# Kernel optimization log

Measured on AMD Instinct MI355X. Metric: run time of the kernel, lower is better.

Reference implementation:

```python
import jax, jax.numpy as jnp
import numpy as np

DIM = 64
WIDTH = 128
INPUT_DIM = 16
N_NODES = 50000
N_EDGES = 100000
N_GRAPHS = 2500
STEPS = 5


def setup_inputs() -> dict:
    key = jax.random.key(0)
    ks = jax.random.split(key, 24)
    d = DIM
    def nrm(i, shape, fan_in):
        return jax.random.normal(ks[i], shape, jnp.float32) / np.float32(np.sqrt(fan_in))
    return {
        "x": jax.random.normal(ks[0], (N_NODES, INPUT_DIM - 1), jnp.float32),
        "z": jax.random.normal(ks[1], (N_NODES,), jnp.float32),
        "edge_attr": jax.random.uniform(ks[2], (N_EDGES, 5), jnp.float32),
        "lin0_w": nrm(3, (INPUT_DIM, d), INPUT_DIM),
        "lin0_b": jnp.zeros((d,), jnp.float32),
        "emlp_w1": nrm(4, (5, WIDTH), 5),
        "emlp_b1": jnp.zeros((WIDTH,), jnp.float32),
        "emlp_w2": nrm(5, (WIDTH, d * d), WIDTH),
        "emlp_b2": jnp.zeros((d * d,), jnp.float32),
        "conv_root": nrm(6, (d, d), d),
        "conv_bias": jnp.zeros((d,), jnp.float32),
        "gru_wi": nrm(7, (3 * d, d), d),
        "gru_wh": nrm(8, (3 * d, d), d),
        "gru_bi": jnp.zeros((3 * d,), jnp.float32),
        "gru_bh": jnp.zeros((3 * d,), jnp.float32),
        "lstm_wi": nrm(9, (4 * d, 2 * d), 2 * d),
        "lstm_wh": nrm(10, (4 * d, d), d),
        "lstm_bi": jnp.zeros((4 * d,), jnp.float32),
        "lstm_bh": jnp.zeros((4 * d,), jnp.float32),
        "lin1_w": nrm(11, (2 * d, d), 2 * d),
        "lin1_b": jnp.zeros((d,), jnp.float32),
        "lin2_w": nrm(12, (d, 1), d),
        "lin2_b": jnp.zeros((1,), jnp.float32),
        "edge_index": jax.random.randint(ks[13], (2, N_EDGES), 0, N_NODES),
        "batch": jnp.sort(jax.random.randint(ks[14], (N_NODES,), 0, N_GRAPHS)),
        "num_graphs": N_GRAPHS,
    }


def reference(x, z, edge_attr, lin0_w, lin0_b, emlp_w1, emlp_b1, emlp_w2, emlp_b2,
              conv_root, conv_bias, gru_wi, gru_wh, gru_bi, gru_bh,
              lstm_wi, lstm_wh, lstm_bi, lstm_bh, lin1_w, lin1_b, lin2_w, lin2_b,
              edge_index, batch, num_graphs):
    d = lin0_w.shape[1]
    n = x.shape[0]
    src, dst = edge_index[0], edge_index[1]
    # lin0 on [x | z]
    out = jax.nn.relu(jnp.concatenate([x, z[:, None]], axis=-1) @ lin0_w + lin0_b)  # [N, d]
    h = out
    # edge MLP -> per-edge weight matrix [E, d, d] (edge_attr fixed, compute once)
    ew = (jax.nn.relu(edge_attr @ emlp_w1 + emlp_b1) @ emlp_w2 + emlp_b2).reshape(-1, d, d)
    deg = jax.ops.segment_sum(jnp.ones_like(src, jnp.float32), dst, num_segments=n)
    denom = jnp.maximum(deg, 1.0)[:, None]
    for _ in range(STEPS):
        # NNConv: gather-matmul-scatter(mean) + root transform + bias
        msg = jnp.einsum('ei,eio->eo', out[src], ew)  # [E, d]
        aggr = jax.ops.segment_sum(msg, dst, num_segments=n) / denom
        m = jax.nn.relu(aggr + out @ conv_root + conv_bias)
        # GRU cell (torch gate order r, z, n)
        gi = m @ gru_wi.T + gru_bi
        gh = h @ gru_wh.T + gru_bh
        i_r, i_z, i_n = jnp.split(gi, 3, axis=-1)
        h_r, h_z, h_n = jnp.split(gh, 3, axis=-1)
        r = jax.nn.sigmoid(i_r + h_r)
        zg = jax.nn.sigmoid(i_z + h_z)
        ng = jnp.tanh(i_n + r * h_n)
        h = (1.0 - zg) * ng + zg * h
        out = h
    # Set2Set pooling (LSTM(2d -> d), torch gate order i, f, g, o)
    B = num_graphs
    q_star = jnp.zeros((B, 2 * d), out.dtype)
    hh = jnp.zeros((B, d), out.dtype)
    cc = jnp.zeros((B, d), out.dtype)
    for _ in range(STEPS):
        g = q_star @ lstm_wi.T + lstm_bi + hh @ lstm_wh.T + lstm_bh
        gi_, gf_, gg_, go_ = jnp.split(g, 4, axis=-1)
        cc = jax.nn.sigmoid(gf_) * cc + jax.nn.sigmoid(gi_) * jnp.tanh(gg_)
        hh = jax.nn.sigmoid(go_) * jnp.tanh(cc)
        q = hh
        e = jnp.sum(out * q[batch], axis=-1)  # [N]
        emax = jax.ops.segment_max(e, batch, num_segments=B)
        a = jnp.exp(e - emax[batch])
        asum = jax.ops.segment_sum(a, batch, num_segments=B) + 1e-16
        a = a / asum[batch]
        r_pool = jax.ops.segment_sum(a[:, None] * out, batch, num_segments=B)  # [B, d]
        q_star = jnp.concatenate([q, r_pool], axis=-1)
    y = jax.nn.relu(q_star @ lin1_w + lin1_b) @ lin2_w + lin2_b
    return y.reshape(-1)
```

## Files before the change

### kernel.cpp

```cpp
#include <hip/hip_runtime.h>
#include <hip/hip_bf16.h>

#define NN 50000
#define NE 100000
#define NG 2500
#define WW 128
#define EPAD 100096
#define KCH 264

typedef _Float16 h8 __attribute__((ext_vector_type(8)));
typedef _Float16 h4 __attribute__((ext_vector_type(4)));
typedef float    f4 __attribute__((ext_vector_type(4)));

#define GLOAD_LDS16(g, l) __builtin_amdgcn_global_load_lds( \
    (const __attribute__((address_space(1))) void*)(g),     \
    (__attribute__((address_space(3))) void*)(l), 16, 0, 0)

__device__ __forceinline__ float sigf(float x) { return 1.0f / (1.0f + __expf(-x)); }

__global__ void k_zero4(float4* __restrict__ p, int n4) {
    int i = blockIdx.x * 256 + threadIdx.x;
    if (i < n4) p[i] = make_float4(0.f, 0.f, 0.f, 0.f);
}

__global__ void k_transpose(float* dst, const float* src, int rows, int cols) {
    int idx = blockIdx.x * 256 + threadIdx.x;
    if (idx >= rows * cols) return;
    int r = idx / cols, c = idx % cols;
    dst[c * rows + r] = src[idx];
}

__global__ void k_lin0(const float* __restrict__ x, const float* __restrict__ z,
                       const float* __restrict__ w, const float* __restrict__ b,
                       float* __restrict__ s) {
    int idx = blockIdx.x * 256 + threadIdx.x;
    int n = idx >> 6, o = idx & 63;
    float acc = b[o];
#pragma unroll
    for (int i = 0; i < 15; i++) acc += x[n * 15 + i] * w[i * 64 + o];
    acc += z[n] * w[15 * 64 + o];
    s[idx] = fmaxf(acc, 0.0f);
}

__global__ void k_deg(const int* __restrict__ dstI, float* __restrict__ deg) {
    int e = blockIdx.x * 256 + threadIdx.x;
    if (e < NE) atomicAdd(&deg[dstI[e]], 1.0f);
}

__global__ void k_s16(const float* __restrict__ s, _Float16* __restrict__ s16) {
    int i = blockIdx.x * 256 + threadIdx.x;
    float4 v = ((const float4*)s)[i];
    h4 o = { (_Float16)v.x, (_Float16)v.y, (_Float16)v.z, (_Float16)v.w };
    *((h4*)s16 + i) = o;
}

__global__ void k_gstart(const int* __restrict__ batch, int* __restrict__ gstart) {
    int n = blockIdx.x * 256 + threadIdx.x;
    if (n > NN) return;
    int b1 = (n < NN) ? batch[n] : NG;
    int b0 = (n == 0) ? -1 : batch[n - 1];
    for (int g = b0 + 1; g <= b1; g++) gstart[g] = n;
}

__global__ void k_emlp_t(const float* __restrict__ ea, const float* __restrict__ w1,
                         const float* __restrict__ b1, _Float16* __restrict__ hidT4) {
    __shared__ _Float16 hl[132][64];
    int t = threadIdx.x;
    int e0 = blockIdx.x * 64;
    int e_l = t & 63, w = t >> 6;
    int e = e0 + e_l;
    float a0 = 0, a1 = 0, a2 = 0, a3 = 0, a4 = 0;
    if (e < NE) {
        a0 = ea[e * 5 + 0]; a1 = ea[e * 5 + 1]; a2 = ea[e * 5 + 2];
        a3 = ea[e * 5 + 3]; a4 = ea[e * 5 + 4];
    }
    for (int h = w * 32; h < w * 32 + 32; h++) {
        float acc = b1[h];
        acc += a0 * w1[0 * 128 + h] + a1 * w1[1 * 128 + h] + a2 * w1[2 * 128 + h]
             + a3 * w1[3 * 128 + h] + a4 * w1[4 * 128 + h];
        hl[h][e_l] = (_Float16)fmaxf(acc, 0.0f);
    }
    if (t < 64) hl[128][t] = (_Float16)1.0f;
    else if (t < 128) hl[129][t - 64] = (_Float16)0.0f;
    else if (t < 192) hl[130][t - 128] = (_Float16)0.0f;
    else hl[131][t - 192] = (_Float16)0.0f;
    __syncthreads();
#pragma unroll
    for (int it = 0; it < 9; it++) {
        int hq = it * 4 + w;
        if (hq < 33) {
            h4 v = { hl[hq * 4 + 0][e_l], hl[hq * 4 + 1][e_l],
                     hl[hq * 4 + 2][e_l], hl[hq * 4 + 3][e_l] };
            *(h4*)(hidT4 + ((size_t)hq * EPAD + e0 + e_l) * 4) = v;
        }
    }
}

__global__ void k_prep_B(const float* __restrict__ w2, const float* __restrict__ b2,
                         _Float16* __restrict__ Bp) {
    int g = blockIdx.x * 256 + threadIdx.x;
    int l = g & 63, tt = (g >> 6) & 3, c = g >> 8;
    int n = tt * 16 + (l & 15);
    int kb = c * 32 + (l >> 4) * 8;
    h8 v;
#pragma unroll
    for (int j = 0; j < 8; j++) {
        int k = kb + j;
        float f = 0.0f;
        if (k < 8192) f = w2[(size_t)k * 64 + n];
        else if (k < 8256) f = b2[(k - 8192) * 64 + n];
        v[j] = (_Float16)f;
    }
    *((h8*)Bp + g) = v;
}

__global__ void k_prep_W(const float* __restrict__ conv_root,
                         const float* __restrict__ gru_wi,
                         const float* __restrict__ gru_wh,
                         _Float16* __restrict__ Bw) {
    int g = blockIdx.x * 256 + threadIdx.x;
    if (g >= 56 * 64) return;
    int l = g & 63, unit = g >> 6;
    int kb = ((unit & 1) * 32) + (l >> 4) * 8;
    h8 v;
    if (unit < 8) {
        int nt = unit >> 1;
        int n = nt * 16 + (l & 15);
#pragma unroll
        for (int j = 0; j < 8; j++) v[j] = (_Float16)conv_root[(kb + j) * 64 + n];
    } else if (unit < 32) {
        int nt = (unit - 8) >> 1;
        int o = nt * 16 + (l & 15);
#pragma unroll
        for (int j = 0; j < 8; j++) v[j] = (_Float16)gru_wi[o * 64 + kb + j];
    } else {
        int nt = (unit - 32) >> 1;
        int o = nt * 16 + (l & 15);
#pragma unroll
        for (int j = 0; j < 8; j++) v[j] = (_Float16)gru_wh[o * 64 + kb + j];
    }
    *((h8*)Bw + g) = v;
}

__global__ __launch_bounds__(256, 3) void k_fused(
        const _Float16* __restrict__ s16, const _Float16* __restrict__ hidT4,
        const _Float16* __restrict__ Bp, const int* __restrict__ srcI,
        const int* __restrict__ dstI, float* __restrict__ aggr) {
    __shared__ uint4 Bl[2][1024];
    int t = threadIdx.x, w = t >> 6, lane = t & 63;
    int m = lane & 15, q = lane >> 4;
    int ew0 = blockIdx.x * 256 + w * 64;

    h8 sA[4][2];
#pragma unroll
    for (int mt = 0; mt < 4; mt++) {
        int e = ew0 + mt * 16 + m;
        int src = (e < NE) ? srcI[e] : 0;
        const _Float16* sp = s16 + (size_t)src * 64;
        sA[mt][0] = *(const h8*)(sp + q * 8);
        sA[mt][1] = *(const h8*)(sp + 32 + q * 8);
    }
    f4 acc[4][4];
#pragma unroll
    for (int mt = 0; mt < 4; mt++)
#pragma unroll
        for (int nt = 0; nt < 4; nt++) acc[mt][nt] = (f4){0.f, 0.f, 0.f, 0.f};

    const h4* hT = (const h4*)hidT4;
    h4 hfA[4], hfB[4];
#pragma unroll
    for (int mt = 0; mt < 4; mt++)
        hfA[mt] = hT[(size_t)0 * EPAD + ew0 + mt * 16 + m];

    {
        const uint4* bs = (const uint4*)Bp;
#pragma unroll
        for (int r = 0; r < 4; r++) GLOAD_LDS16(bs + r * 256 + t, &Bl[0][r * 256 + t]);
    }
    __syncthreads();

#define COMPUTE_STEP(BUF, HH)                                                  \
    _Pragma("unroll")                                                          \
    for (int c2 = 0; c2 < 4; c2++) {                                           \
        h8 b0 = *(const h8*)&Bl[BUF][(c2 * 4 + 0) * 64 + lane];                \
        h8 b1 = *(const h8*)&Bl[BUF][(c2 * 4 + 1) * 64 + lane];                \
        h8 b2 = *(const h8*)&Bl[BUF][(c2 * 4 + 2) * 64 + lane];                \
        h8 b3 = *(const h8*)&Bl[BUF][(c2 * 4 + 3) * 64 + lane];                \
        _Pragma("unroll")                                                      \
        for (int mt = 0; mt < 4; mt++) {                                       \
            h8 a = sA[mt][c2 & 1] * hfA[mt][(HH) + (c2 >> 1)];                 \
            acc[mt][0] = __builtin_amdgcn_mfma_f32_16x16x32_f16(a, b0, acc[mt][0], 0, 0, 0); \
            acc[mt][1] = __builtin_amdgcn_mfma_f32_16x16x32_f16(a, b1, acc[mt][1], 0, 0, 0); \
            acc[mt][2] = __builtin_amdgcn_mfma_f32_16x16x32_f16(a, b2, acc[mt][2], 0, 0, 0); \
            acc[mt][3] = __builtin_amdgcn_mfma_f32_16x16x32_f16(a, b3, acc[mt][3], 0, 0, 0); \
        }                                                                      \
    }

    for (int tt = 0; tt < 33; tt++) {
        {
            const uint4* bs = (const uint4*)Bp + (size_t)(2 * tt + 1) * 1024;
#pragma unroll
            for (int r = 0; r < 4; r++) GLOAD_LDS16(bs + r * 256 + t, &Bl[1][r * 256 + t]);
        }
        {
#pragma unroll
            for (int mt = 0; mt < 4; mt++)
                hfB[mt] = hT[(size_t)(tt + 1) * EPAD + ew0 + mt * 16 + m];
        }
        COMPUTE_STEP(0, 0)
        __syncthreads();

        if (tt + 1 < 33) {
            const uint4* bs = (const uint4*)Bp + (size_t)(2 * tt + 2) * 1024;
#pragma unroll
            for (int r = 0; r < 4; r++) GLOAD_LDS16(bs + r * 256 + t, &Bl[0][r * 256 + t]);
        }
        COMPUTE_STEP(1, 2)
#pragma unroll
        for (int mt = 0; mt < 4; mt++) hfA[mt] = hfB[mt];
        __syncthreads();
    }
#undef COMPUTE_STEP

#pragma unroll
    for (int mt = 0; mt < 4; mt++) {
        int eb = ew0 + mt * 16 + q * 4;
#pragma unroll
        for (int r = 0; r < 4; r++) {
            int e = eb + r;
            if (e < NE) {
                int d = dstI[e];
                float* ap = aggr + (size_t)d * 64 + m;
                atomicAdd(ap + 0,  acc[mt][0][r]);
                atomicAdd(ap + 16, acc[mt][1][r]);
                atomicAdd(ap + 32, acc[mt][2][r]);
                atomicAdd(ap + 48, acc[mt][3][r]);
            }
        }
    }
}

__global__ __launch_bounds__(256) void k_combine2(
        float* __restrict__ s, _Float16* __restrict__ s16,
        const float* __restrict__ aggr, const float* __restrict__ deg,
        const _Float16* __restrict__ Bw, const float* __restrict__ cb,
        const float* __restrict__ bi, const float* __restrict__ bh) {
    __shared__ _Float16 ml[4][16][72];
    int t = threadIdx.x, w = t >> 6, lane = t & 63;
    int m = lane & 15, q = lane >> 4;
    int nb = blockIdx.x * 64 + w * 16;

    h8 sa0, sa1;
    {
        int node = nb + m; if (node >= NN) node = NN - 1;
        const _Float16* sp = s16 + (size_t)node * 64;
        sa0 = *(const h8*)(sp + q * 8);
        sa1 = *(const h8*)(sp + 32 + q * 8);
    }
    const h8* BW = (const h8*)Bw;

    f4 X[4], GH[12];
#pragma unroll
    for (int nt = 0; nt < 4; nt++) {
        X[nt] = (f4){0.f, 0.f, 0.f, 0.f};
        X[nt] = __builtin_amdgcn_mfma_f32_16x16x32_f16(sa0, BW[(nt * 2 + 0) * 64 + lane], X[nt], 0, 0, 0);
        X[nt] = __builtin_amdgcn_mfma_f32_16x16x32_f16(sa1, BW[(nt * 2 + 1) * 64 + lane], X[nt], 0, 0, 0);
    }
#pragma unroll
    for (int nt = 0; nt < 12; nt++) {
        GH[nt] = (f4){0.f, 0.f, 0.f, 0.f};
        GH[nt] = __builtin_amdgcn_mfma_f32_16x16x32_f16(sa0, BW[(32 + nt * 2 + 0) * 64 + lane], GH[nt], 0, 0, 0);
        GH[nt] = __builtin_amdgcn_mfma_f32_16x16x32_f16(sa1, BW[(32 + nt * 2 + 1) * 64 + lane], GH[nt], 0, 0, 0);
    }
#pragma unroll
    for (int r = 0; r < 4; r++) {
        int node = nb + q * 4 + r; if (node >= NN) node = NN - 1;
        float dn = fmaxf(deg[node], 1.0f);
#pragma unroll
        for (int nt = 0; nt < 4; nt++) {
            int o = nt * 16 + m;
            float mv = X[nt][r] + aggr[(size_t)node * 64 + o] / dn + cb[o];
            ml[w][q * 4 + r][o] = (_Float16)fmaxf(mv, 0.0f);
        }
    }
    __syncthreads();
    h8 ma0 = *(const h8*)&ml[w][m][q * 8];
    h8 ma1 = *(const h8*)&ml[w][m][32 + q * 8];

    f4 GI[12];
#pragma unroll
    for (int nt = 0; nt < 12; nt++) {
        GI[nt] = (f4){0.f, 0.f, 0.f, 0.f};
        GI[nt] = __builtin_amdgcn_mfma_f32_16x16x32_f16(ma0, BW[(8 + nt * 2 + 0) * 64 + lane], GI[nt], 0, 0, 0);
        GI[nt] = __builtin_amdgcn_mfma_f32_16x16x32_f16(ma1, BW[(8 + nt * 2 + 1) * 64 + lane], GI[nt], 0, 0, 0);
    }
#pragma unroll
    for (int og = 0; og < 4; og++) {
        int o = og * 16 + m;
        float bir = bi[o],       bhr = bh[o];
        float biz = bi[64 + o],  bhz = bh[64 + o];
        float bin = bi[128 + o], bhn = bh[128 + o];
#pragma unroll
        for (int r = 0; r < 4; r++) {
            int node = nb + q * 4 + r;
            if (node >= NN) continue;
            float rr = sigf(GI[og][r] + bir + GH[og][r] + bhr);
            float zz = sigf(GI[4 + og][r] + biz + GH[4 + og][r] + bhz);
            float ng = tanhf(GI[8 + og][r] + bin + rr * (GH[8 + og][r] + bhn));
            float hold = s[(size_t)node * 64 + o];
            float hnew = (1.0f - zz) * ng + zz * hold;
            s[(size_t)node * 64 + o] = hnew;
            s16[(size_t)node * 64 + o] = (_Float16)hnew;
        }
    }
}

__global__ void k_s2s(float* __restrict__ q_star, float* __restrict__ hh,
                      float* __restrict__ cc, const float* __restrict__ LiT,
                      const float* __restrict__ LhT, const float* __restrict__ bi,
                      const float* __restrict__ bh, const float* __restrict__ s,
                      const int* __restrict__ gstart, float* __restrict__ e_v) {
    __shared__ float qs[128], hv[64], g[256], qn[64];
    int b = blockIdx.x, t = threadIdx.x;
    if (t < 128) qs[t] = q_star[b * 128 + t];
    else if (t < 192) hv[t - 128] = hh[b * 64 + t - 128];
    __syncthreads();
    float acc = bi[t] + bh[t];
    for (int k = 0; k < 128; k++) acc += qs[k] * LiT[k * 256 + t];
    for (int k = 0; k < 64; k++) acc += hv[k] * LhT[k * 256 + t];
    g[t] = acc;
    __syncthreads();
    if (t < 64) {
        float c_new = sigf(g[64 + t]) * cc[b * 64 + t] + sigf(g[t]) * tanhf(g[128 + t]);
        cc[b * 64 + t] = c_new;
        float hq = sigf(g[192 + t]) * tanhf(c_new);
        hh[b * 64 + t] = hq;
        qn[t] = hq;
        q_star[b * 128 + t] = hq;
    }
    __syncthreads();
    if (t >= 64) return;
    int o = t;
    int n0 = gstart[b], n1 = gstart[b + 1];
    float q = qn[o];
    float mx = -3.4e38f;
    for (int n = n0; n < n1; n++) {
        float v = s[(size_t)n * 64 + o] * q;
#pragma unroll
        for (int off = 32; off; off >>= 1) v += __shfl_xor(v, off, 64);
        if (o == 0) e_v[n] = v;
        mx = fmaxf(mx, v);
    }
    float asum = 0.0f, rp = 0.0f;
    for (int n = n0; n < n1; n++) {
        float a = __expf(e_v[n] - mx);
        asum += a;
        rp += a * s[(size_t)n * 64 + o];
    }
    q_star[b * 128 + 64 + o] = rp / (asum + 1e-16f);
}

__global__ void k_final(const float* __restrict__ q_star, const float* __restrict__ w1,
                        const float* __restrict__ b1, const float* __restrict__ w2,
                        const float* __restrict__ b2, float* __restrict__ y) {
    __shared__ float qs[128];
    int b = blockIdx.x, t = threadIdx.x;
    qs[t] = q_star[b * 128 + t];
    qs[64 + t] = q_star[b * 128 + 64 + t];
    __syncthreads();
    float acc = b1[t];
    for (int k = 0; k < 128; k++) acc += qs[k] * w1[k * 64 + t];
    float hid = fmaxf(acc, 0.0f) * w2[t];
#pragma unroll
    for (int off = 32; off; off >>= 1) hid += __shfl_down(hid, off, 64);
    if (t == 0) y[b] = hid + b2[0];
}

static inline void zero_f(float* p, size_t nfloats, hipStream_t stream) {
    int n4 = (int)(nfloats / 4);
    k_zero4<<<(n4 + 255) / 256, 256, 0, stream>>>((float4*)p, n4);
}

extern "C" void kernel_launch(void* const* d_in, const int* in_sizes, int n_in,
                              void* d_out, int out_size, void* d_ws, size_t ws_size,
                              hipStream_t stream) {
    const float* x       = (const float*)d_in[0];
    const float* z       = (const float*)d_in[1];
    const float* ea      = (const float*)d_in[2];
    const float* lin0_w  = (const float*)d_in[3];
    const float* lin0_b  = (const float*)d_in[4];
    const float* emlp_w1 = (const float*)d_in[5];
    const float* emlp_b1 = (const float*)d_in[6];
    const float* emlp_w2 = (const float*)d_in[7];
    const float* emlp_b2 = (const float*)d_in[8];
    const float* conv_r  = (const float*)d_in[9];
    const float* conv_b  = (const float*)d_in[10];
    const float* gru_wi  = (const float*)d_in[11];
    const float* gru_wh  = (const float*)d_in[12];
    const float* gru_bi  = (const float*)d_in[13];
    const float* gru_bh  = (const float*)d_in[14];
    const float* lstm_wi = (const float*)d_in[15];
    const float* lstm_wh = (const float*)d_in[16];
    const float* lstm_bi = (const float*)d_in[17];
    const float* lstm_bh = (const float*)d_in[18];
    const float* lin1_w  = (const float*)d_in[19];
    const float* lin1_b  = (const float*)d_in[20];
    const float* lin2_w  = (const float*)d_in[21];
    const float* lin2_b  = (const float*)d_in[22];
    const int* eidx      = (const int*)d_in[23];
    const int* batch     = (const int*)d_in[24];
    const int* srcI = eidx;
    const int* dstI = eidx + NE;
    float* y = (float*)d_out;

    char* w = (char*)d_ws;
    size_t off = 0;
    auto alloc = [&](size_t bytes) -> void* {
        void* p = w + off;
        off += (bytes + 255) & ~(size_t)255;
        return p;
    };
    float* s      = (float*)alloc((size_t)NN * 64 * 4);
    float* aggr   = (float*)alloc((size_t)NN * 64 * 4);
    float* deg    = (float*)alloc((size_t)NN * 4);
    float* e_v    = (float*)alloc((size_t)NN * 4);
    float* q_star = (float*)alloc((size_t)NG * 128 * 4);
    float* hh     = (float*)alloc((size_t)NG * 64 * 4);
    float* cc     = (float*)alloc((size_t)NG * 64 * 4);
    float* LiT    = (float*)alloc(256 * 128 * 4);
    float* LhT    = (float*)alloc(256 * 64 * 4);
    int*   gstart = (int*)alloc((size_t)(NG + 1) * 4);
    _Float16* s16 = (_Float16*)alloc((size_t)NN * 64 * 2);
    _Float16* hidT= (_Float16*)alloc((size_t)34 * EPAD * 4 * 2);
    _Float16* Bp  = (_Float16*)alloc((size_t)KCH * 4 * 64 * 8 * 2);
    _Float16* Bw  = (_Float16*)alloc((size_t)56 * 64 * 8 * 2);
    (void)ws_size;

    k_transpose<<<(256 * 128 + 255) / 256, 256, 0, stream>>>(LiT, lstm_wi, 256, 128);
    k_transpose<<<(256 * 64 + 255) / 256, 256, 0, stream>>>(LhT, lstm_wh, 256, 64);
    k_prep_W<<<14, 256, 0, stream>>>(conv_r, gru_wi, gru_wh, Bw);

    k_lin0<<<NN * 64 / 256, 256, 0, stream>>>(x, z, lin0_w, lin0_b, s);
    k_s16<<<NN * 16 / 256, 256, 0, stream>>>(s, s16);
    zero_f(deg, NN, stream);
    k_deg<<<(NE + 255) / 256, 256, 0, stream>>>(dstI, deg);
    k_gstart<<<(NN + 256) / 256, 256, 0, stream>>>(batch, gstart);
    k_emlp_t<<<EPAD / 64, 256, 0, stream>>>(ea, emlp_w1, emlp_b1, hidT);
    k_prep_B<<<KCH * 4 * 64 / 256, 256, 0, stream>>>(emlp_w2, emlp_b2, Bp);

    for (int step = 0; step < 5; step++) {
        zero_f(aggr, (size_t)NN * 64, stream);
        k_fused<<<EPAD / 256, 256, 0, stream>>>(s16, hidT, Bp, srcI, dstI, aggr);
        k_combine2<<<(NN + 63) / 64, 256, 0, stream>>>(s, s16, aggr, deg, Bw,
                                                       conv_b, gru_bi, gru_bh);
    }

    zero_f(q_star, (size_t)NG * 128 + NG * 64 + NG * 64, stream);
    for (int it = 0; it < 5; it++) {
        k_s2s<<<NG, 256, 0, stream>>>(q_star, hh, cc, LiT, LhT, lstm_bi, lstm_bh,
                                      s, gstart, e_v);
    }
    k_final<<<NG, 64, 0, stream>>>(q_star, lin1_w, lin1_b, lin2_w, lin2_b, y);
}
```

Before: 993.9 us.

## Fuse Set2Set iterations and final MLP, fold fp16 cast and aggr zeroing

Merges the five Set2Set launches and the final MLP into one per-graph kernel that keeps LSTM state in shared memory, which removes the q_star/hh/cc global buffers and eleven launches. lin0 writes the fp16 copy directly, so the separate conversion kernel is gone. combine2 zeroes aggr after reading it, so the per-step zero kernel is replaced by a single zero before the loop. Together these cut launch overhead and redundant memory passes. The cost is an extra store per aggr element in combine2 and a long-running per-graph block.

```diff
diff --git a/kernel.cpp b/kernel.cpp
--- a/kernel.cpp
+++ b/kernel.cpp
@@ -32,26 +32,21 @@
 
 __global__ void k_lin0(const float* __restrict__ x, const float* __restrict__ z,
                        const float* __restrict__ w, const float* __restrict__ b,
-                       float* __restrict__ s) {
+                       float* __restrict__ s, _Float16* __restrict__ s16) {
     int idx = blockIdx.x * 256 + threadIdx.x;
     int n = idx >> 6, o = idx & 63;
     float acc = b[o];
 #pragma unroll
     for (int i = 0; i < 15; i++) acc += x[n * 15 + i] * w[i * 64 + o];
     acc += z[n] * w[15 * 64 + o];
-    s[idx] = fmaxf(acc, 0.0f);
+    float r = fmaxf(acc, 0.0f);
+    s[idx] = r;
+    s16[idx] = (_Float16)r;
 }
 
 __global__ void k_deg(const int* __restrict__ dstI, float* __restrict__ deg) {
     int e = blockIdx.x * 256 + threadIdx.x;
     if (e < NE) atomicAdd(&deg[dstI[e]], 1.0f);
-}
-
-__global__ void k_s16(const float* __restrict__ s, _Float16* __restrict__ s16) {
-    int i = blockIdx.x * 256 + threadIdx.x;
-    float4 v = ((const float4*)s)[i];
-    h4 o = { (_Float16)v.x, (_Float16)v.y, (_Float16)v.z, (_Float16)v.w };
-    *((h4*)s16 + i) = o;
 }
 
 __global__ void k_gstart(const int* __restrict__ batch, int* __restrict__ gstart) {
@@ -242,7 +237,7 @@
 
 __global__ __launch_bounds__(256) void k_combine2(
         float* __restrict__ s, _Float16* __restrict__ s16,
-        const float* __restrict__ aggr, const float* __restrict__ deg,
+        float* __restrict__ aggr, const float* __restrict__ deg,
         const _Float16* __restrict__ Bw, const float* __restrict__ cb,
         const float* __restrict__ bi, const float* __restrict__ bh) {
     __shared__ _Float16 ml[4][16][72];
@@ -274,12 +269,17 @@
     }
 #pragma unroll
     for (int r = 0; r < 4; r++) {
-        int node = nb + q * 4 + r; if (node >= NN) node = NN - 1;
-        float dn = fmaxf(deg[node], 1.0f);
+        int node = nb + q * 4 + r;
+        bool ok = node < NN;
+        int nc = ok ? node : NN - 1;
+        float dn = fmaxf(deg[nc], 1.0f);
 #pragma unroll
         for (int nt = 0; nt < 4; nt++) {
             int o = nt * 16 + m;
-            float mv = X[nt][r] + aggr[(size_t)node * 64 + o] / dn + cb[o];
+            size_t ai = (size_t)nc * 64 + o;
+            float av = aggr[ai];
+            if (ok) aggr[ai] = 0.0f;
+            float mv = X[nt][r] + av / dn + cb[o];
             ml[w][q * 4 + r][o] = (_Float16)fmaxf(mv, 0.0f);
         }
     }
@@ -315,65 +315,62 @@
     }
 }
 
-__global__ void k_s2s(float* __restrict__ q_star, float* __restrict__ hh,
-                      float* __restrict__ cc, const float* __restrict__ LiT,
-                      const float* __restrict__ LhT, const float* __restrict__ bi,
-                      const float* __restrict__ bh, const float* __restrict__ s,
-                      const int* __restrict__ gstart, float* __restrict__ e_v) {
-    __shared__ float qs[128], hv[64], g[256], qn[64];
+__global__ void k_s2s5(const float* __restrict__ LiT, const float* __restrict__ LhT,
+                       const float* __restrict__ bi, const float* __restrict__ bh,
+                       const float* __restrict__ s, const int* __restrict__ gstart,
+                       float* __restrict__ e_v,
+                       const float* __restrict__ w1, const float* __restrict__ b1,
+                       const float* __restrict__ w2, const float* __restrict__ b2,
+                       float* __restrict__ y) {
+    __shared__ float qs[128], hv[64], cv[64], g[256], qn[64];
     int b = blockIdx.x, t = threadIdx.x;
-    if (t < 128) qs[t] = q_star[b * 128 + t];
-    else if (t < 192) hv[t - 128] = hh[b * 64 + t - 128];
+    if (t < 128) qs[t] = 0.0f;
+    if (t < 64) { hv[t] = 0.0f; cv[t] = 0.0f; }
     __syncthreads();
-    float acc = bi[t] + bh[t];
-    for (int k = 0; k < 128; k++) acc += qs[k] * LiT[k * 256 + t];
-    for (int k = 0; k < 64; k++) acc += hv[k] * LhT[k * 256 + t];
-    g[t] = acc;
-    __syncthreads();
+    int n0 = gstart[b], n1 = gstart[b + 1];
+
+    for (int it = 0; it < 5; it++) {
+        float acc = bi[t] + bh[t];
+        for (int k = 0; k < 128; k++) acc += qs[k] * LiT[k * 256 + t];
+        for (int k = 0; k < 64; k++) acc += hv[k] * LhT[k * 256 + t];
+        g[t] = acc;
+        __syncthreads();
+        if (t < 64) {
+            float c_new = sigf(g[64 + t]) * cv[t] + sigf(g[t]) * tanhf(g[128 + t]);
+            cv[t] = c_new;
+            float hq = sigf(g[192 + t]) * tanhf(c_new);
+            hv[t] = hq;
+            qn[t] = hq;
+            qs[t] = hq;
+            int o = t;
+            float qv = qn[o];
+            float mx = -3.4e38f;
+            for (int n = n0; n < n1; n++) {
+                float v = s[(size_t)n * 64 + o] * qv;
+#pragma unroll
+                for (int off = 32; off; off >>= 1) v += __shfl_xor(v, off, 64);
+                if (o == 0) e_v[n] = v;
+                mx = fmaxf(mx, v);
+            }
+            float asum = 0.0f, rp = 0.0f;
+            for (int n = n0; n < n1; n++) {
+                float a = __expf(e_v[n] - mx);
+                asum += a;
+                rp += a * s[(size_t)n * 64 + o];
+            }
+            qs[64 + o] = rp / (asum + 1e-16f);
+        }
+        __syncthreads();
+    }
+
     if (t < 64) {
-        float c_new = sigf(g[64 + t]) * cc[b * 64 + t] + sigf(g[t]) * tanhf(g[128 + t]);
-        cc[b * 64 + t] = c_new;
-        float hq = sigf(g[192 + t]) * tanhf(c_new);
-        hh[b * 64 + t] = hq;
-        qn[t] = hq;
-        q_star[b * 128 + t] = hq;
-    }
-    __syncthreads();
-    if (t >= 64) return;
-    int o = t;
-    int n0 = gstart[b], n1 = gstart[b + 1];
-    float q = qn[o];
-    float mx = -3.4e38f;
-    for (int n = n0; n < n1; n++) {
-        float v = s[(size_t)n * 64 + o] * q;
-#pragma unroll
-        for (int off = 32; off; off >>= 1) v += __shfl_xor(v, off, 64);
-        if (o == 0) e_v[n] = v;
-        mx = fmaxf(mx, v);
-    }
-    float asum = 0.0f, rp = 0.0f;
-    for (int n = n0; n < n1; n++) {
-        float a = __expf(e_v[n] - mx);
-        asum += a;
-        rp += a * s[(size_t)n * 64 + o];
-    }
-    q_star[b * 128 + 64 + o] = rp / (asum + 1e-16f);
-}
-
-__global__ void k_final(const float* __restrict__ q_star, const float* __restrict__ w1,
-                        const float* __restrict__ b1, const float* __restrict__ w2,
-                        const float* __restrict__ b2, float* __restrict__ y) {
-    __shared__ float qs[128];
-    int b = blockIdx.x, t = threadIdx.x;
-    qs[t] = q_star[b * 128 + t];
-    qs[64 + t] = q_star[b * 128 + 64 + t];
-    __syncthreads();
-    float acc = b1[t];
-    for (int k = 0; k < 128; k++) acc += qs[k] * w1[k * 64 + t];
-    float hid = fmaxf(acc, 0.0f) * w2[t];
-#pragma unroll
-    for (int off = 32; off; off >>= 1) hid += __shfl_down(hid, off, 64);
-    if (t == 0) y[b] = hid + b2[0];
+        float acc = b1[t];
+        for (int k = 0; k < 128; k++) acc += qs[k] * w1[k * 64 + t];
+        float hid = fmaxf(acc, 0.0f) * w2[t];
+#pragma unroll
+        for (int off = 32; off; off >>= 1) hid += __shfl_down(hid, off, 64);
+        if (t == 0) y[b] = hid + b2[0];
+    }
 }
 
 static inline void zero_f(float* p, size_t nfloats, hipStream_t stream) {
@@ -424,9 +421,6 @@
     float* aggr   = (float*)alloc((size_t)NN * 64 * 4);
     float* deg    = (float*)alloc((size_t)NN * 4);
     float* e_v    = (float*)alloc((size_t)NN * 4);
-    float* q_star = (float*)alloc((size_t)NG * 128 * 4);
-    float* hh     = (float*)alloc((size_t)NG * 64 * 4);
-    float* cc     = (float*)alloc((size_t)NG * 64 * 4);
     float* LiT    = (float*)alloc(256 * 128 * 4);
     float* LhT    = (float*)alloc(256 * 64 * 4);
     int*   gstart = (int*)alloc((size_t)(NG + 1) * 4);
@@ -440,25 +434,20 @@
     k_transpose<<<(256 * 64 + 255) / 256, 256, 0, stream>>>(LhT, lstm_wh, 256, 64);
     k_prep_W<<<14, 256, 0, stream>>>(conv_r, gru_wi, gru_wh, Bw);
 
-    k_lin0<<<NN * 64 / 256, 256, 0, stream>>>(x, z, lin0_w, lin0_b, s);
-    k_s16<<<NN * 16 / 256, 256, 0, stream>>>(s, s16);
+    k_lin0<<<NN * 64 / 256, 256, 0, stream>>>(x, z, lin0_w, lin0_b, s, s16);
     zero_f(deg, NN, stream);
     k_deg<<<(NE + 255) / 256, 256, 0, stream>>>(dstI, deg);
     k_gstart<<<(NN + 256) / 256, 256, 0, stream>>>(batch, gstart);
     k_emlp_t<<<EPAD / 64, 256, 0, stream>>>(ea, emlp_w1, emlp_b1, hidT);
     k_prep_B<<<KCH * 4 * 64 / 256, 256, 0, stream>>>(emlp_w2, emlp_b2, Bp);
+    zero_f(aggr, (size_t)NN * 64, stream);
 
     for (int step = 0; step < 5; step++) {
-        zero_f(aggr, (size_t)NN * 64, stream);
         k_fused<<<EPAD / 256, 256, 0, stream>>>(s16, hidT, Bp, srcI, dstI, aggr);
         k_combine2<<<(NN + 63) / 64, 256, 0, stream>>>(s, s16, aggr, deg, Bw,
                                                        conv_b, gru_bi, gru_bh);
     }
 
-    zero_f(q_star, (size_t)NG * 128 + NG * 64 + NG * 64, stream);
-    for (int it = 0; it < 5; it++) {
-        k_s2s<<<NG, 256, 0, stream>>>(q_star, hh, cc, LiT, LhT, lstm_bi, lstm_bh,
-                                      s, gstart, e_v);
-    }
-    k_final<<<NG, 64, 0, stream>>>(q_star, lin1_w, lin1_b, lin2_w, lin2_b, y);
-}
+    k_s2s5<<<NG, 256, 0, stream>>>(LiT, LhT, lstm_bi, lstm_bh, s, gstart, e_v,
+                                   lin1_w, lin1_b, lin2_w, lin2_b, y);
+}
```

Result: slower. 1.070 ms (+7.7%).
